# Optimization experiments

Hardware: AMD Instinct MI355X
Metric: run time of the kernel (lower is better)

The kernel has to match this reference:

```python
import jax, jax.numpy as jnp
import numpy as np

B, L, D, H = 1, 320, 128, 4
DH = D // H
LN_EPS = 1e-5


def setup_inputs() -> dict:
    key = jax.random.key(0)
    ks = jax.random.split(key, 4)
    z = jax.random.normal(ks[0], (B, L, L, D), jnp.float32)
    mask = jax.random.randint(ks[1], (B, L), 0, 2).astype(jnp.int32)
    ln_g = jnp.ones((D,), jnp.float32)
    ln_b = jnp.zeros((D,), jnp.float32)
    w_qkv = (jax.random.normal(ks[2], (3 * D, D), jnp.float32) * 0.02)
    b_qkv = jnp.zeros((3 * D,), jnp.float32)
    w_out = (jax.random.normal(ks[3], (D, D), jnp.float32) * 0.02)
    b_out = jnp.zeros((D,), jnp.float32)
    return {"z": z, "mask": mask, "ln_g": ln_g, "ln_b": ln_b,
            "w_qkv": w_qkv, "b_qkv": b_qkv, "w_out": w_out, "b_out": b_out}


def reference(z, mask, ln_g, ln_b, w_qkv, b_qkv, w_out, b_out):
    # z: (B, L, L, D), mask: (B, L) with 1 = keep, 0 = masked key
    mu = jnp.mean(z, axis=-1, keepdims=True)
    var = jnp.mean(jnp.square(z - mu), axis=-1, keepdims=True)
    zn = (z - mu) * jax.lax.rsqrt(var + LN_EPS) * ln_g + ln_b

    zf = zn.reshape(B * L, L, D)                       # row-wise: each of B*L rows is a length-L sequence
    qkv = zf @ w_qkv.T + b_qkv                         # (B*L, L, 3D)
    q, k, v = jnp.split(qkv, 3, axis=-1)

    def split_heads(x):
        return x.reshape(B * L, L, H, DH).transpose(0, 2, 1, 3)  # (B*L, H, L, DH)

    q, k, v = split_heads(q), split_heads(k), split_heads(v)
    scores = jnp.einsum('nhqd,nhkd->nhqk', q, k) / np.sqrt(DH).astype(np.float32)

    # additive -inf at masked key positions, shared across all L rows of a batch
    bias = jnp.where(mask > 0, 0.0, -jnp.inf).astype(scores.dtype)   # (B, L)
    bias = jnp.repeat(bias, L, axis=0)[:, None, None, :]             # (B*L, 1, 1, L)

    attn = jax.nn.softmax(scores + bias, axis=-1)
    o = jnp.einsum('nhqk,nhkd->nhqd', attn, v)
    o = o.transpose(0, 2, 1, 3).reshape(B * L, L, D)
    out = o @ w_out.T + b_out
    return z + out.reshape(B, L, L, D)
```

## Files before the change

### kernel.cpp

```cpp
#include <hip/hip_runtime.h>

#define LQ 320
#define NSEQ 320
#define NROWS (NSEQ*LQ)
#define DDIM 128
#define NH 4
#define DHD 32
#define LN_EPS 1e-5f
#define QSC2 0.25508652025545527f

typedef __bf16 bf16x8 __attribute__((ext_vector_type(8)));
typedef __bf16 bf16x2 __attribute__((ext_vector_type(2)));
typedef float f32x4 __attribute__((ext_vector_type(4)));
union FragU { unsigned int u[4]; bf16x8 v; };

__device__ int g_inv[LQ];
__device__ int g_cnt;
__device__ __align__(16) unsigned short g_wbf[512 * DDIM];

__device__ inline unsigned short f2bf(float f) {
    return __builtin_bit_cast(unsigned short, (__bf16)f);
}
__device__ inline unsigned int pack2(float a, float b) {
    bf16x2 t;
    t[0] = (__bf16)a;
    t[1] = (__bf16)b;
    return __builtin_bit_cast(unsigned int, t);
}

__global__ __launch_bounds__(256) void k0_ln(
    const float* __restrict__ z, const float* __restrict__ ln_g, const float* __restrict__ ln_b,
    unsigned int* __restrict__ znws, const int* __restrict__ mask,
    const float* __restrict__ w_qkv, const float* __restrict__ w_out)
{
    const int tid = threadIdx.x;
    const int bx = blockIdx.x;
    const int rowbase = bx * 64;
    const int lane = tid & 63;
    const int wid = tid >> 6;

    if (bx == 0) {
        if (tid < 64) {
            int carry = 0;
            #pragma unroll 1
            for (int c = 0; c < 5; ++c) {
                const int i = c * 64 + tid;
                const int m = (mask[i] > 0) ? 1 : 0;
                int v = m;
                #pragma unroll
                for (int off = 1; off < 64; off <<= 1) {
                    const int o = __shfl_up(v, off, 64);
                    if (tid >= off) v += o;
                }
                v += carry;
                if (m) g_inv[v - 1] = i;
                carry = __shfl(v, 63, 64);
            }
            if (tid == 0) g_cnt = carry;
            for (int s = carry + tid; s < LQ; s += 64) g_inv[s] = 0;
        }
    } else if (bx <= 32) {
        const int cid = (bx - 1) * 256 + tid;
        const int l2  = cid & 63;
        const int nt  = (cid >> 6) & 7;
        const int kt  = (cid >> 9) & 3;
        const int s4  = cid >> 11;
        const int qn2 = l2 & 15, gd2 = l2 >> 4;
        const int row = s4 * 128 + nt * 16 + qn2;
        const float4* src4 = (s4 < 3) ? (const float4*)w_qkv : (const float4*)w_out;
        const int rloc = (s4 < 3) ? row : (row - 384);
        const int fi = rloc * 32 + kt * 8 + gd2 * 2;
        const float4 a = src4[fi];
        const float4 b = src4[fi + 1];
        uint4 val;
        val.x = pack2(a.x, a.y);
        val.y = pack2(a.z, a.w);
        val.z = pack2(b.x, b.y);
        val.w = pack2(b.z, b.w);
        ((uint4*)g_wbf)[cid] = val;
    }

    const float g0 = ln_g[2 * lane], g1 = ln_g[2 * lane + 1];
    const float bb0 = ln_b[2 * lane], bb1 = ln_b[2 * lane + 1];
    #pragma unroll 1
    for (int r = wid; r < 64; r += 4) {
        const int row = rowbase + r;
        const float2 v = *(const float2*)(z + (size_t)row * DDIM + 2 * lane);
        float s = v.x + v.y;
        float s2 = v.x * v.x + v.y * v.y;
        #pragma unroll
        for (int off = 32; off > 0; off >>= 1) {
            s  += __shfl_xor(s, off, 64);
            s2 += __shfl_xor(s2, off, 64);
        }
        const float mu = s * (1.0f / 128.0f);
        const float var = s2 * (1.0f / 128.0f) - mu * mu;
        const float rs = rsqrtf(var + LN_EPS);
        znws[(size_t)row * 64 + lane] =
            pack2((v.x - mu) * rs * g0 + bb0, (v.y - mu) * rs * g1 + bb1);
    }
}

__global__ __launch_bounds__(256, 4) void k1_qkv(
    const unsigned short* __restrict__ znws, const float* __restrict__ b_qkv,
    unsigned short* __restrict__ qws, unsigned short* __restrict__ kws,
    unsigned short* __restrict__ vws)
{
    __shared__ unsigned short ldsb[17408];
    const int tid = threadIdx.x;
    const int bx = blockIdx.x;
    const int sect = bx % 3;
    const int mbase = (bx / 3) * 128;
    const int lane = tid & 63;
    const int wid = tid >> 6;
    const int qn = lane & 15, gd = lane >> 4;

    const int cnt = __builtin_amdgcn_readfirstlane(g_cnt);
    const int PT16 = (cnt + 15) & ~15;
    const int CP8  = (cnt + 7) & ~7;
    const int stride = (sect == 0) ? LQ : ((sect == 1) ? PT16 : CP8);
    const int rows_total = NSEQ * stride;
    if (mbase >= rows_total) return;

    {
        const uint4* src = (const uint4*)g_wbf + sect * 2048;
        uint4* dst = (uint4*)ldsb;
        #pragma unroll
        for (int i = 0; i < 8; ++i) dst[tid + i * 256] = src[tid + i * 256];
    }

    const int n0 = mbase / stride;
    const int s0 = mbase - n0 * stride;

    int arow[2];
    #pragma unroll
    for (int rg = 0; rg < 2; ++rg) {
        const int off = wid * 32 + rg * 16 + qn;
        int n = n0, s = s0 + off;
        while (s >= stride) { s -= stride; ++n; }
        int grow = n * LQ + ((sect == 0) ? s : g_inv[s]);
        if (mbase + off >= rows_total) grow = 0;
        arow[rg] = grow;
    }

    __syncthreads();

    const f32x4 zero4 = {0.f, 0.f, 0.f, 0.f};
    f32x4 acc[2][8];
    #pragma unroll
    for (int rg = 0; rg < 2; ++rg)
        #pragma unroll
        for (int nt = 0; nt < 8; ++nt) acc[rg][nt] = zero4;

    #pragma unroll
    for (int kt = 0; kt < 4; ++kt) {
        FragU af[2];
        #pragma unroll
        for (int rg = 0; rg < 2; ++rg)
            af[rg].v = *(const bf16x8*)&znws[(size_t)arow[rg] * DDIM + kt * 32 + gd * 8];
        #pragma unroll
        for (int nt = 0; nt < 8; ++nt) {
            FragU bf;
            bf.v = *(const bf16x8*)&ldsb[((kt * 8 + nt) * 64 + lane) * 8];
            #pragma unroll
            for (int rg = 0; rg < 2; ++rg)
                acc[rg][nt] = __builtin_amdgcn_mfma_f32_16x16x32_bf16(af[rg].v, bf.v, acc[rg][nt], 0, 0, 0);
        }
    }

    float bq[8];
    #pragma unroll
    for (int nt = 0; nt < 8; ++nt) bq[nt] = b_qkv[sect * 128 + nt * 16 + qn];
    const float sc = (sect == 0) ? QSC2 : 1.0f;

    __syncthreads();
    unsigned short* tr = ldsb;

    if (sect < 2) {
        #pragma unroll
        for (int rg = 0; rg < 2; ++rg) {
            #pragma unroll
            for (int r = 0; r < 4; ++r) {
                const int row = wid * 32 + rg * 16 + 4 * gd + r;
                #pragma unroll
                for (int nt = 0; nt < 8; ++nt) {
                    const int col = nt * 16 + qn;
                    tr[row * 132 + col] = f2bf((acc[rg][nt][r] + bq[nt]) * sc);
                }
            }
        }
    } else {
        #pragma unroll
        for (int rg = 0; rg < 2; ++rg) {
            const int row0 = wid * 32 + rg * 16 + 4 * gd;
            #pragma unroll
            for (int nt = 0; nt < 8; ++nt) {
                const int col = nt * 16 + qn;
                uint2 pv;
                pv.x = pack2(acc[rg][nt][0] + bq[nt], acc[rg][nt][1] + bq[nt]);
                pv.y = pack2(acc[rg][nt][2] + bq[nt], acc[rg][nt][3] + bq[nt]);
                *(uint2*)&tr[col * 132 + row0] = pv;
            }
        }
    }
    __syncthreads();

    if (sect < 2) {
        unsigned short* dst = (sect == 0) ? qws : kws;
        #pragma unroll 1
        for (int k16 = 0; k16 < 16; ++k16) {
            const int o2 = lane * 4 + k16 * 256;
            const int i_loc = o2 >> 5, d = o2 & 31;
            if (mbase + i_loc < rows_total) {
                int n = n0, s = s0 + i_loc;
                while (s >= stride) { s -= stride; ++n; }
                const ushort4 val = *(const ushort4*)&tr[i_loc * 132 + wid * 32 + d];
                *(ushort4*)&dst[((size_t)(n * NH + wid) * LQ + s) * DHD + d] = val;
            }
        }
    } else {
        #pragma unroll 1
        for (int k16 = 0; k16 < 16; ++k16) {
            const int o2 = lane * 4 + k16 * 256;
            const int d = o2 >> 7, i_loc = o2 & 127;
            if (mbase + i_loc < rows_total) {
                int n = n0, s = s0 + i_loc;
                while (s >= stride) { s -= stride; ++n; }
                const ushort4 val = *(const ushort4*)&tr[(wid * 32 + d) * 132 + i_loc];
                *(ushort4*)&vws[(size_t)(n * NH + wid) * (DHD * LQ) + d * CP8 + s] = val;
            }
        }
    }
}

#define KSTR 20
__global__ __launch_bounds__(256, 4) void k2_attn_mfma(
    const unsigned short* __restrict__ qws, const unsigned short* __restrict__ kws,
    const unsigned short* __restrict__ vtws, unsigned short* __restrict__ ows)
{
    __shared__ unsigned int kT[LQ * KSTR];
    const int tid = threadIdx.x;
    const int bx = blockIdx.x;
    const int nh = bx / 5;
    const int qs = bx - nh * 5;
    const int lane = tid & 63;
    const int wid = tid >> 6;
    const int qn = lane & 15;
    const int gd = lane >> 4;

    const int cnt = __builtin_amdgcn_readfirstlane(g_cnt);
    const int PT  = (cnt + 15) & ~15;
    const int CP8 = (cnt + 7) & ~7;
    const int NCH = (PT + 159) / 160;

    const uint4* kp4 = (const uint4*)(kws + (size_t)nh * LQ * DHD);
    #pragma unroll 1
    for (int idx = tid; idx < PT * 4; idx += 256) {
        const int r = idx >> 2, c4 = idx & 3;
        *(uint4*)&kT[r * KSTR + 4 * c4] = kp4[idx];
    }
    __syncthreads();

    const f32x4 zero4 = {0.f, 0.f, 0.f, 0.f};
    const int alo = (((gd & 1) << 5) | qn) << 2;
    const int ahi = alo + 64;
    const bool hiT = (gd >= 2);
    const int n = nh >> 2, h = nh & 3;
    const unsigned short* vbase = vtws + (size_t)nh * DHD * LQ;

    const int qt = qs * 4 + wid;

    FragU qf;
    qf.v = *(const bf16x8*)(qws + ((size_t)nh * LQ + qt * 16 + qn) * DHD + 8 * gd);

    f32x4 o0 = zero4, o1 = zero4;
    float m_run = -1e30f;
    float l_run = 0.f;

    #pragma unroll 1
    for (int ch = 0; ch < NCH; ++ch) {
        const int tb = ch * 10;

        FragU vf0[5], vf1[5];
        #pragma unroll
        for (int kc = 0; kc < 5; ++kc) {
            if ((tb + 2 * kc) * 16 < cnt) {
                const int koff = ch * 160 + 32 * kc + 8 * gd;
                vf0[kc].v = *(const bf16x8*)(vbase + (size_t)qn * CP8 + koff);
                vf1[kc].v = *(const bf16x8*)(vbase + (size_t)(16 + qn) * CP8 + koff);
            }
        }

        f32x4 st[10];
        #pragma unroll
        for (int kt = 0; kt < 10; ++kt) {
            const int ktg = tb + kt;
            if (ktg * 16 < cnt) {
                FragU kf;
                const uint4 kv = *(const uint4*)&kT[(ktg * 16 + qn) * KSTR + 4 * gd];
                kf.u[0] = kv.x; kf.u[1] = kv.y; kf.u[2] = kv.z; kf.u[3] = kv.w;
                f32x4 c0 = zero4;
                if ((ktg + 1) * 16 > cnt) {
                    const int jb = ktg * 16 + 4 * gd;
                    #pragma unroll
                    for (int r = 0; r < 4; ++r)
                        c0[r] = (jb + r < cnt) ? 0.f : -1e30f;
                }
                st[kt] = __builtin_amdgcn_mfma_f32_16x16x32_bf16(kf.v, qf.v, c0, 0, 0, 0);
            }
        }

        float mh = -1e30f;
        #pragma unroll
        for (int kt = 0; kt < 10; ++kt)
            if ((tb + kt) * 16 < cnt)
                mh = fmaxf(mh, fmaxf(fmaxf(st[kt][0], st[kt][1]), fmaxf(st[kt][2], st[kt][3])));
        mh = fmaxf(mh, __shfl_xor(mh, 16, 64));
        mh = fmaxf(mh, __shfl_xor(mh, 32, 64));
        const float m_new = fmaxf(m_run, mh);
        const float scl = __builtin_amdgcn_exp2f(m_run - m_new);
        m_run = m_new;
        l_run *= scl;
        o0 *= scl;
        o1 *= scl;

        float ls0 = 0.f, ls1 = 0.f;
        #pragma unroll
        for (int kt = 0; kt < 10; ++kt) {
            if ((tb + kt) * 16 < cnt) {
                st[kt][0] = __builtin_amdgcn_exp2f(st[kt][0] - m_new);
                st[kt][1] = __builtin_amdgcn_exp2f(st[kt][1] - m_new);
                st[kt][2] = __builtin_amdgcn_exp2f(st[kt][2] - m_new);
                st[kt][3] = __builtin_amdgcn_exp2f(st[kt][3] - m_new);
                ls0 += st[kt][0] + st[kt][1];
                ls1 += st[kt][2] + st[kt][3];
            } else {
                st[kt] = zero4;
            }
        }
        l_run += ls0 + ls1;

        #pragma unroll
        for (int kc = 0; kc < 5; ++kc) {
            if ((tb + 2 * kc) * 16 < cnt) {
                const int t0 = 2 * kc, t1 = 2 * kc + 1;
                const unsigned int p01a = pack2(st[t0][0], st[t0][1]);
                const unsigned int p23a = pack2(st[t0][2], st[t0][3]);
                const unsigned int p01b = pack2(st[t1][0], st[t1][1]);
                const unsigned int p23b = pack2(st[t1][2], st[t1][3]);
                FragU pa;
                {
                    const int a0 = __builtin_amdgcn_ds_bpermute(alo, (int)p01a);
                    const int b0 = __builtin_amdgcn_ds_bpermute(alo, (int)p01b);
                    const int a1 = __builtin_amdgcn_ds_bpermute(alo, (int)p23a);
                    const int b1 = __builtin_amdgcn_ds_bpermute(alo, (int)p23b);
                    const int a2 = __builtin_amdgcn_ds_bpermute(ahi, (int)p01a);
                    const int b2 = __builtin_amdgcn_ds_bpermute(ahi, (int)p01b);
                    const int a3 = __builtin_amdgcn_ds_bpermute(ahi, (int)p23a);
                    const int b3 = __builtin_amdgcn_ds_bpermute(ahi, (int)p23b);
                    pa.u[0] = (unsigned int)(hiT ? b0 : a0);
                    pa.u[1] = (unsigned int)(hiT ? b1 : a1);
                    pa.u[2] = (unsigned int)(hiT ? b2 : a2);
                    pa.u[3] = (unsigned int)(hiT ? b3 : a3);
                }
                o0 = __builtin_amdgcn_mfma_f32_16x16x32_bf16(pa.v, vf0[kc].v, o0, 0, 0, 0);
                o1 = __builtin_amdgcn_mfma_f32_16x16x32_bf16(pa.v, vf1[kc].v, o1, 0, 0, 0);
            }
        }
    }

    l_run += __shfl_xor(l_run, 16, 64);
    l_run += __shfl_xor(l_run, 32, 64);
    const float inv = 1.0f / l_run;

    #pragma unroll
    for (int r = 0; r < 4; ++r) {
        const int qg = qt * 16 + 4 * gd + r;
        unsigned short* orow = ows + ((size_t)(n * LQ + qg)) * DDIM + h * DHD + qn;
        orow[0]  = f2bf(o0[r] * inv);
        orow[16] = f2bf(o1[r] * inv);
    }
}

__global__ __launch_bounds__(256, 4) void k3_out(
    const unsigned short* __restrict__ ows,
    const float* __restrict__ b_out, const float* __restrict__ z,
    float* __restrict__ out)
{
    __shared__ unsigned short ldsb[16384];
    const int tid = threadIdx.x;
    const int mbase = blockIdx.x * 128;
    const int lane = tid & 63;
    const int wid = tid >> 6;
    const int qn = lane & 15, gd = lane >> 4;

    {
        const uint4* src = (const uint4*)g_wbf + 3 * 2048;
        uint4* dst = (uint4*)ldsb;
        #pragma unroll
        for (int i = 0; i < 8; ++i) dst[tid + i * 256] = src[tid + i * 256];
    }
    __syncthreads();

    const f32x4 zero4 = {0.f, 0.f, 0.f, 0.f};
    f32x4 acc[2][8];
    #pragma unroll
    for (int rg = 0; rg < 2; ++rg)
        #pragma unroll
        for (int nt = 0; nt < 8; ++nt) acc[rg][nt] = zero4;

    #pragma unroll
    for (int kt = 0; kt < 4; ++kt) {
        FragU af[2];
        #pragma unroll
        for (int rg = 0; rg < 2; ++rg)
            af[rg].v = *(const bf16x8*)&ows[
                (size_t)(mbase + wid * 32 + rg * 16 + qn) * DDIM + kt * 32 + gd * 8];
        #pragma unroll
        for (int nt = 0; nt < 8; ++nt) {
            FragU bf;
            bf.v = *(const bf16x8*)&ldsb[((kt * 8 + nt) * 64 + lane) * 8];
            #pragma unroll
            for (int rg = 0; rg < 2; ++rg)
                acc[rg][nt] = __builtin_amdgcn_mfma_f32_16x16x32_bf16(af[rg].v, bf.v, acc[rg][nt], 0, 0, 0);
        }
    }

    float bb[8];
    #pragma unroll
    for (int nt = 0; nt < 8; ++nt) bb[nt] = b_out[nt * 16 + qn];

    #pragma unroll
    for (int rg = 0; rg < 2; ++rg) {
        #pragma unroll
        for (int r = 0; r < 4; ++r) {
            const int grow = mbase + wid * 32 + rg * 16 + 4 * gd + r;
            const float* zr = z + (size_t)grow * DDIM;
            float* outr = out + (size_t)grow * DDIM;
            #pragma unroll
            for (int nt = 0; nt < 8; ++nt) {
                const int cg = nt * 16 + qn;
                outr[cg] = acc[rg][nt][r] + bb[nt] + zr[cg];
            }
        }
    }
}

extern "C" void kernel_launch(void* const* d_in, const int* in_sizes, int n_in,
                              void* d_out, int out_size, void* d_ws, size_t ws_size,
                              hipStream_t stream) {
    const float* z     = (const float*)d_in[0];
    const int*   mask  = (const int*)d_in[1];
    const float* ln_g  = (const float*)d_in[2];
    const float* ln_b  = (const float*)d_in[3];
    const float* w_qkv = (const float*)d_in[4];
    const float* b_qkv = (const float*)d_in[5];
    const float* w_out = (const float*)d_in[6];
    const float* b_out = (const float*)d_in[7];
    float* out = (float*)d_out;

    unsigned short* ws = (unsigned short*)d_ws;
    const size_t qE = (size_t)NSEQ * NH * LQ * DHD;
    unsigned short* qws = ws;
    unsigned short* kws = qws + qE;
    unsigned short* vws = kws + qE;
    unsigned short* shared_rgn = vws + qE;
    unsigned int*   znws = (unsigned int*)shared_rgn;
    unsigned short* ows  = shared_rgn;

    hipLaunchKernelGGL(k0_ln, dim3(NROWS / 64), dim3(256), 0, stream,
                       z, ln_g, ln_b, znws, mask, w_qkv, w_out);
    hipLaunchKernelGGL(k1_qkv, dim3(2400), dim3(256), 0, stream,
                       (const unsigned short*)znws, b_qkv, qws, kws, vws);
    hipLaunchKernelGGL(k2_attn_mfma, dim3(6400), dim3(256), 0, stream,
                       qws, kws, vws, ows);
    hipLaunchKernelGGL(k3_out, dim3(800), dim3(256), 0, stream,
                       ows, b_out, z, out);
}
```

Baseline: 207.8 us.

## Rewrite attention kernel with 32x32x16 MFMA tiles and permlane32 swaps

The attention kernel moves from 16x16x32 MFMA tiles with a K tile staged in LDS to 32x32x16 MFMA tiles. K and V fragments are read straight from global memory, with no LDS staging and no block barrier. The P operand is rearranged with v_permlane32_swap instead of eight ds_bpermute calls per chunk. The online softmax skips the rescale when the new max exceeds the running max by no more than 8, which adds exp2 range risk. Each block now has 5 waves and handles 32 query rows per wave, and K padding becomes a multiple of 32 in the QKV kernel.

```diff
diff --git a/kernel.cpp b/kernel.cpp
--- a/kernel.cpp
+++ b/kernel.cpp
@@ -12,6 +12,7 @@
 typedef __bf16 bf16x8 __attribute__((ext_vector_type(8)));
 typedef __bf16 bf16x2 __attribute__((ext_vector_type(2)));
 typedef float f32x4 __attribute__((ext_vector_type(4)));
+typedef float f32x16 __attribute__((ext_vector_type(16)));
 union FragU { unsigned int u[4]; bf16x8 v; };
 
 __device__ int g_inv[LQ];
@@ -26,6 +27,9 @@
     t[0] = (__bf16)a;
     t[1] = (__bf16)b;
     return __builtin_bit_cast(unsigned int, t);
+}
+__device__ inline void pl32swap(unsigned int &a, unsigned int &b) {
+    asm volatile("v_permlane32_swap_b32 %0, %1" : "+v"(a), "+v"(b));
 }
 
 __global__ __launch_bounds__(256) void k0_ln(
@@ -116,9 +120,9 @@
     const int qn = lane & 15, gd = lane >> 4;
 
     const int cnt = __builtin_amdgcn_readfirstlane(g_cnt);
-    const int PT16 = (cnt + 15) & ~15;
+    const int PT32 = (cnt + 31) & ~31;
     const int CP8  = (cnt + 7) & ~7;
-    const int stride = (sect == 0) ? LQ : ((sect == 1) ? PT16 : CP8);
+    const int stride = (sect == 0) ? LQ : ((sect == 1) ? PT32 : CP8);
     const int rows_total = NSEQ * stride;
     if (mbase >= rows_total) return;
 
@@ -233,152 +237,103 @@
     }
 }
 
-#define KSTR 20
-__global__ __launch_bounds__(256, 4) void k2_attn_mfma(
+__global__ __launch_bounds__(320, 4) void k2_attn_mfma(
     const unsigned short* __restrict__ qws, const unsigned short* __restrict__ kws,
     const unsigned short* __restrict__ vtws, unsigned short* __restrict__ ows)
 {
-    __shared__ unsigned int kT[LQ * KSTR];
     const int tid = threadIdx.x;
     const int bx = blockIdx.x;
-    const int nh = bx / 5;
-    const int qs = bx - nh * 5;
+    const int nh = bx >> 1;
     const int lane = tid & 63;
     const int wid = tid >> 6;
-    const int qn = lane & 15;
-    const int gd = lane >> 4;
+    const int qt = (bx & 1) * 5 + wid;
+    const int qc = lane & 31;
+    const int hf = lane >> 5;
 
     const int cnt = __builtin_amdgcn_readfirstlane(g_cnt);
-    const int PT  = (cnt + 15) & ~15;
-    const int CP8 = (cnt + 7) & ~7;
-    const int NCH = (PT + 159) / 160;
-
-    const uint4* kp4 = (const uint4*)(kws + (size_t)nh * LQ * DHD);
+    const int PT32 = (cnt + 31) & ~31;
+    const int CP8  = (cnt + 7) & ~7;
+    const int NT   = PT32 >> 5;
+
+    const int n = nh >> 2, h = nh & 3;
+    const unsigned short* kb = kws + (size_t)nh * LQ * DHD + hf * 8;
+    const unsigned short* vb = vtws + (size_t)nh * DHD * LQ + (size_t)qc * CP8 + hf * 8;
+    const unsigned short* qp = qws + ((size_t)nh * LQ + qt * 32 + qc) * DHD + hf * 8;
+
+    FragU qf1, qf2;
+    qf1.v = *(const bf16x8*)qp;
+    qf2.v = *(const bf16x8*)(qp + 16);
+
+    f32x16 o;
+    #pragma unroll
+    for (int r = 0; r < 16; ++r) o[r] = 0.f;
+    float m_run = -1e30f, l_run = 0.f;
+
     #pragma unroll 1
-    for (int idx = tid; idx < PT * 4; idx += 256) {
-        const int r = idx >> 2, c4 = idx & 3;
-        *(uint4*)&kT[r * KSTR + 4 * c4] = kp4[idx];
-    }
-    __syncthreads();
-
-    const f32x4 zero4 = {0.f, 0.f, 0.f, 0.f};
-    const int alo = (((gd & 1) << 5) | qn) << 2;
-    const int ahi = alo + 64;
-    const bool hiT = (gd >= 2);
-    const int n = nh >> 2, h = nh & 3;
-    const unsigned short* vbase = vtws + (size_t)nh * DHD * LQ;
-
-    const int qt = qs * 4 + wid;
-
-    FragU qf;
-    qf.v = *(const bf16x8*)(qws + ((size_t)nh * LQ + qt * 16 + qn) * DHD + 8 * gd);
-
-    f32x4 o0 = zero4, o1 = zero4;
-    float m_run = -1e30f;
-    float l_run = 0.f;
-
-    #pragma unroll 1
-    for (int ch = 0; ch < NCH; ++ch) {
-        const int tb = ch * 10;
-
-        FragU vf0[5], vf1[5];
-        #pragma unroll
-        for (int kc = 0; kc < 5; ++kc) {
-            if ((tb + 2 * kc) * 16 < cnt) {
-                const int koff = ch * 160 + 32 * kc + 8 * gd;
-                vf0[kc].v = *(const bf16x8*)(vbase + (size_t)qn * CP8 + koff);
-                vf1[kc].v = *(const bf16x8*)(vbase + (size_t)(16 + qn) * CP8 + koff);
-            }
-        }
-
-        f32x4 st[10];
-        #pragma unroll
-        for (int kt = 0; kt < 10; ++kt) {
-            const int ktg = tb + kt;
-            if (ktg * 16 < cnt) {
-                FragU kf;
-                const uint4 kv = *(const uint4*)&kT[(ktg * 16 + qn) * KSTR + 4 * gd];
-                kf.u[0] = kv.x; kf.u[1] = kv.y; kf.u[2] = kv.z; kf.u[3] = kv.w;
-                f32x4 c0 = zero4;
-                if ((ktg + 1) * 16 > cnt) {
-                    const int jb = ktg * 16 + 4 * gd;
-                    #pragma unroll
-                    for (int r = 0; r < 4; ++r)
-                        c0[r] = (jb + r < cnt) ? 0.f : -1e30f;
-                }
-                st[kt] = __builtin_amdgcn_mfma_f32_16x16x32_bf16(kf.v, qf.v, c0, 0, 0, 0);
-            }
-        }
-
-        float mh = -1e30f;
-        #pragma unroll
-        for (int kt = 0; kt < 10; ++kt)
-            if ((tb + kt) * 16 < cnt)
-                mh = fmaxf(mh, fmaxf(fmaxf(st[kt][0], st[kt][1]), fmaxf(st[kt][2], st[kt][3])));
-        mh = fmaxf(mh, __shfl_xor(mh, 16, 64));
+    for (int kt = 0; kt < NT; ++kt) {
+        const unsigned short* kr = kb + (size_t)(kt * 32 + qc) * DHD;
+        FragU kf1, kf2, vf1, vf2;
+        kf1.v = *(const bf16x8*)kr;
+        kf2.v = *(const bf16x8*)(kr + 16);
+        vf1.v = *(const bf16x8*)(vb + kt * 32);
+        vf2.v = *(const bf16x8*)(vb + kt * 32 + 16);
+
+        f32x16 c0;
+        #pragma unroll
+        for (int r = 0; r < 16; ++r) c0[r] = 0.f;
+        if ((kt + 1) * 32 > cnt) {
+            #pragma unroll
+            for (int r = 0; r < 16; ++r) {
+                const int krow = kt * 32 + (r & 3) + 8 * (r >> 2) + 4 * hf;
+                c0[r] = (krow < cnt) ? 0.f : -1e30f;
+            }
+        }
+        f32x16 st = __builtin_amdgcn_mfma_f32_32x32x16_bf16(kf1.v, qf1.v, c0, 0, 0, 0);
+        st = __builtin_amdgcn_mfma_f32_32x32x16_bf16(kf2.v, qf2.v, st, 0, 0, 0);
+
+        float mh = st[0];
+        #pragma unroll
+        for (int r = 1; r < 16; ++r) mh = fmaxf(mh, st[r]);
         mh = fmaxf(mh, __shfl_xor(mh, 32, 64));
-        const float m_new = fmaxf(m_run, mh);
-        const float scl = __builtin_amdgcn_exp2f(m_run - m_new);
-        m_run = m_new;
-        l_run *= scl;
-        o0 *= scl;
-        o1 *= scl;
-
-        float ls0 = 0.f, ls1 = 0.f;
-        #pragma unroll
-        for (int kt = 0; kt < 10; ++kt) {
-            if ((tb + kt) * 16 < cnt) {
-                st[kt][0] = __builtin_amdgcn_exp2f(st[kt][0] - m_new);
-                st[kt][1] = __builtin_amdgcn_exp2f(st[kt][1] - m_new);
-                st[kt][2] = __builtin_amdgcn_exp2f(st[kt][2] - m_new);
-                st[kt][3] = __builtin_amdgcn_exp2f(st[kt][3] - m_new);
-                ls0 += st[kt][0] + st[kt][1];
-                ls1 += st[kt][2] + st[kt][3];
-            } else {
-                st[kt] = zero4;
-            }
-        }
-        l_run += ls0 + ls1;
-
-        #pragma unroll
-        for (int kc = 0; kc < 5; ++kc) {
-            if ((tb + 2 * kc) * 16 < cnt) {
-                const int t0 = 2 * kc, t1 = 2 * kc + 1;
-                const unsigned int p01a = pack2(st[t0][0], st[t0][1]);
-                const unsigned int p23a = pack2(st[t0][2], st[t0][3]);
-                const unsigned int p01b = pack2(st[t1][0], st[t1][1]);
-                const unsigned int p23b = pack2(st[t1][2], st[t1][3]);
-                FragU pa;
-                {
-                    const int a0 = __builtin_amdgcn_ds_bpermute(alo, (int)p01a);
-                    const int b0 = __builtin_amdgcn_ds_bpermute(alo, (int)p01b);
-                    const int a1 = __builtin_amdgcn_ds_bpermute(alo, (int)p23a);
-                    const int b1 = __builtin_amdgcn_ds_bpermute(alo, (int)p23b);
-                    const int a2 = __builtin_amdgcn_ds_bpermute(ahi, (int)p01a);
-                    const int b2 = __builtin_amdgcn_ds_bpermute(ahi, (int)p01b);
-                    const int a3 = __builtin_amdgcn_ds_bpermute(ahi, (int)p23a);
-                    const int b3 = __builtin_amdgcn_ds_bpermute(ahi, (int)p23b);
-                    pa.u[0] = (unsigned int)(hiT ? b0 : a0);
-                    pa.u[1] = (unsigned int)(hiT ? b1 : a1);
-                    pa.u[2] = (unsigned int)(hiT ? b2 : a2);
-                    pa.u[3] = (unsigned int)(hiT ? b3 : a3);
-                }
-                o0 = __builtin_amdgcn_mfma_f32_16x16x32_bf16(pa.v, vf0[kc].v, o0, 0, 0, 0);
-                o1 = __builtin_amdgcn_mfma_f32_16x16x32_bf16(pa.v, vf1[kc].v, o1, 0, 0, 0);
-            }
-        }
-    }
-
-    l_run += __shfl_xor(l_run, 16, 64);
+        if (!__all(mh <= m_run + 8.0f)) {
+            const float m_new = fmaxf(m_run, mh);
+            const float scl = __builtin_amdgcn_exp2f(m_run - m_new);
+            l_run *= scl;
+            #pragma unroll
+            for (int r = 0; r < 16; ++r) o[r] *= scl;
+            m_run = m_new;
+        }
+        #pragma unroll
+        for (int r = 0; r < 16; ++r) st[r] = __builtin_amdgcn_exp2f(st[r] - m_run);
+        l_run += (((st[0] + st[1]) + (st[2] + st[3])) + ((st[4] + st[5]) + (st[6] + st[7])))
+               + (((st[8] + st[9]) + (st[10] + st[11])) + ((st[12] + st[13]) + (st[14] + st[15])));
+
+        unsigned int a01 = pack2(st[0], st[1]), a23 = pack2(st[2], st[3]);
+        unsigned int a45 = pack2(st[4], st[5]), a67 = pack2(st[6], st[7]);
+        pl32swap(a01, a45);
+        pl32swap(a23, a67);
+        FragU pa1;
+        pa1.u[0] = a01; pa1.u[1] = a23; pa1.u[2] = a45; pa1.u[3] = a67;
+        o = __builtin_amdgcn_mfma_f32_32x32x16_bf16(pa1.v, vf1.v, o, 0, 0, 0);
+
+        unsigned int b01 = pack2(st[8], st[9]),  b23 = pack2(st[10], st[11]);
+        unsigned int b45 = pack2(st[12], st[13]), b67 = pack2(st[14], st[15]);
+        pl32swap(b01, b45);
+        pl32swap(b23, b67);
+        FragU pa2;
+        pa2.u[0] = b01; pa2.u[1] = b23; pa2.u[2] = b45; pa2.u[3] = b67;
+        o = __builtin_amdgcn_mfma_f32_32x32x16_bf16(pa2.v, vf2.v, o, 0, 0, 0);
+    }
+
     l_run += __shfl_xor(l_run, 32, 64);
     const float inv = 1.0f / l_run;
 
     #pragma unroll
-    for (int r = 0; r < 4; ++r) {
-        const int qg = qt * 16 + 4 * gd + r;
-        unsigned short* orow = ows + ((size_t)(n * LQ + qg)) * DDIM + h * DHD + qn;
-        orow[0]  = f2bf(o0[r] * inv);
-        orow[16] = f2bf(o1[r] * inv);
+    for (int r = 0; r < 16; ++r) {
+        const int qloc = (r & 3) + 8 * (r >> 2) + 4 * hf;
+        const float iv = __shfl(inv, qloc, 64);
+        const int qg = qt * 32 + qloc;
+        ows[((size_t)(n * LQ + qg)) * DDIM + h * DHD + qc] = f2bf(o[r] * iv);
     }
 }
 
@@ -472,7 +427,7 @@
                        z, ln_g, ln_b, znws, mask, w_qkv, w_out);
     hipLaunchKernelGGL(k1_qkv, dim3(2400), dim3(256), 0, stream,
                        (const unsigned short*)znws, b_qkv, qws, kws, vws);
-    hipLaunchKernelGGL(k2_attn_mfma, dim3(6400), dim3(256), 0, stream,
+    hipLaunchKernelGGL(k2_attn_mfma, dim3(2560), dim3(320), 0, stream,
                        qws, kws, vws, ows);
     hipLaunchKernelGGL(k3_out, dim3(800), dim3(256), 0, stream,
                        ows, b_out, z, out);
```

New measurement: 195.6 us. 5.9% less time.
